# Performance work log

Hardware: AMD Instinct MI355X
Metric: run time of the kernel (lower is better)

The kernel has to match this reference:

```python
import jax, jax.numpy as jnp
import numpy as np

N = 100000
E1 = 600000
E2 = 300000
H = 128
IN = 35
G = 1000
EPS = 1e-5


def _rbf(d):
    # d: [E] distances -> [E, 9] gaussian RBF on [0, 6] with 9 centers
    mu = jnp.linspace(0.0, 6.0, 9, dtype=d.dtype)
    sigma = 6.0 / 9.0
    return jnp.exp(-(((d[:, None] - mu) / sigma) ** 2))


def _bn_eval(x, g, b):
    # BatchNorm1d in eval mode with running_mean=0, running_var=1
    return g * x * (1.0 / np.sqrt(1.0 + EPS)) + b


def _leaky(x):
    return jnp.where(x >= 0, x, 0.01 * x)


def _branch(h, pos, edge_index, cW, cB, nW, nB, g, b):
    row, col = edge_index[0], edge_index[1]
    d = jnp.linalg.norm(pos[row] - pos[col], axis=-1)          # [E]
    radial = jax.nn.silu(_rbf(d) @ cW + cB)                    # [E, H]
    msg = h[row] * radial                                      # gather-mul
    agg = jax.ops.segment_sum(msg, col, num_segments=h.shape[0])  # scatter-add
    return _bn_eval(_leaky((h + agg) @ nW + nB), g, b)


def setup_inputs() -> dict:
    key = jax.random.key(0)
    ks = jax.random.split(key, 16)
    s = lambda fan: 1.0 / np.sqrt(fan)
    inp = {
        "x": jax.random.normal(ks[0], (N, IN), jnp.float32),
        "pos": jax.random.normal(ks[1], (N, 3), jnp.float32) * 2.0,
        "W_in": jax.random.normal(ks[2], (IN, H), jnp.float32) * s(IN),
        "b_in": jnp.zeros((H,), jnp.float32),
        "coordW": jax.random.normal(ks[3], (3, 2, 9, H), jnp.float32) * s(9),
        "coordB": jnp.zeros((3, 2, H), jnp.float32),
        "nodeW": jax.random.normal(ks[4], (3, 2, H, H), jnp.float32) * s(H),
        "nodeB": jnp.zeros((3, 2, H), jnp.float32),
        "bnG": jnp.ones((3, 2, H), jnp.float32),
        "bnB": jnp.zeros((3, 2, H), jnp.float32),
        "fcW": jax.random.normal(ks[5], (3, H, H), jnp.float32) * s(H),
        "fcB": jnp.zeros((3, H), jnp.float32),
        "fcBnG": jnp.ones((3, H), jnp.float32),
        "fcBnB": jnp.zeros((3, H), jnp.float32),
        "outW": jax.random.normal(ks[6], (H, 1), jnp.float32) * s(H),
        "outB": jnp.zeros((1,), jnp.float32),
        "edge_index_intra": jax.random.randint(ks[7], (2, E1), 0, N, jnp.int32),
        "edge_index_inter": jax.random.randint(ks[8], (2, E2), 0, N, jnp.int32),
        "batch": jnp.sort(jax.random.randint(ks[9], (N,), 0, G, jnp.int32)),
    }
    return inp


def reference(x, pos, W_in, b_in, coordW, coordB, nodeW, nodeB, bnG, bnB,
              fcW, fcB, fcBnG, fcBnB, outW, outB,
              edge_index_intra, edge_index_inter, batch):
    h = jax.nn.silu(x @ W_in + b_in)
    for l in range(3):  # 3 GraphInteractionLayers
        intra = _branch(h, pos, edge_index_intra, coordW[l, 0], coordB[l, 0],
                        nodeW[l, 0], nodeB[l, 0], bnG[l, 0], bnB[l, 0])
        inter = _branch(h, pos, edge_index_inter, coordW[l, 1], coordB[l, 1],
                        nodeW[l, 1], nodeB[l, 1], bnG[l, 1], bnB[l, 1])
        h = intra + inter
    hg = jax.ops.segment_sum(h, batch, num_segments=G)  # global_add_pool [G, H]
    for i in range(3):
        hg = _bn_eval(_leaky(hg @ fcW[i] + fcB[i]), fcBnG[i], fcBnB[i])
    out = hg @ outW + outB  # [G, 1]
    return out.reshape(-1)
```

## Files before the change

kernel.cpp:

```cpp
#include <hip/hip_runtime.h>
#include <hip/hip_fp16.h>
#include <math.h>

#define NN   100000
#define HH   128
#define INF_ 35
#define GG   1000
#define LBM  64
#define NBINS 2048
#define DSCALE 128.0f
#define DINV   0.0078125f
#define DCLAMP 15.992f

typedef __attribute__((ext_vector_type(8))) short short8;
typedef __attribute__((ext_vector_type(4))) float f32x4;

static __device__ __forceinline__ float silu_f(float x){ return x / (1.f + __expf(-x)); }
static __device__ __forceinline__ unsigned bf16rne(float x){
    unsigned u = __float_as_uint(x);
    return (u + 0x7FFFu + ((u>>16)&1u)) >> 16;
}
#define BN_INV 0.9999950000374997f

__global__ void k_count(const int* __restrict__ ei1, const int* __restrict__ ei2,
                        int E1, int E2, int n, int* __restrict__ deg){
    int e = blockIdx.x*256 + threadIdx.x;
    int ET = E1 + E2;
    if (e >= ET) return;
    int c;
    if (e < E1) c = ei1[E1 + e];
    else        c = n + ei2[E2 + (e - E1)];
    atomicAdd(&deg[c], 1);
}

__global__ void k_scan1(const int* __restrict__ deg, int n2, int* __restrict__ off, int* __restrict__ bsum){
    __shared__ int s[256];
    int tid = threadIdx.x; int i = blockIdx.x*256 + tid;
    int v = (i<n2)? deg[i] : 0;
    s[tid] = v; __syncthreads();
    for (int ofs=1; ofs<256; ofs<<=1){
        int t = (tid>=ofs)? s[tid-ofs] : 0;
        __syncthreads(); s[tid] += t; __syncthreads();
    }
    if (i<n2) off[i] = s[tid] - v;
    if (tid==255) bsum[blockIdx.x] = s[255];
}

__global__ void k_scan2(int* __restrict__ bsum, int nb){
    __shared__ int s[1024];
    int tid = threadIdx.x;
    int v = (tid<nb)? bsum[tid] : 0;
    s[tid] = v; __syncthreads();
    for (int ofs=1; ofs<1024; ofs<<=1){
        int t = (tid>=ofs)? s[tid-ofs] : 0;
        __syncthreads(); s[tid] += t; __syncthreads();
    }
    if (tid<nb) bsum[tid] = s[tid] - v;
}

__global__ void k_scan3(int* __restrict__ off, const int* __restrict__ bsum, int n2, int ET){
    int i = blockIdx.x*256 + threadIdx.x;
    if (i<n2) off[i] += bsum[i>>8];
    if (i==0) off[n2] = ET;
}

__global__ void k_fill(const int* __restrict__ ei1, const int* __restrict__ ei2,
                       int E1, int E2, int n, const float* __restrict__ pos,
                       const int* __restrict__ off, int* __restrict__ cur,
                       float2* __restrict__ rec){
    int e = blockIdx.x*256 + threadIdx.x;
    int ET = E1 + E2;
    if (e >= ET) return;
    int r, creal, cslot;
    if (e < E1){ r = ei1[e];        creal = ei1[E1 + e];        cslot = creal; }
    else       { int ee = e - E1; r = ei2[ee]; creal = ei2[E2 + ee]; cslot = n + creal; }
    int slot = atomicAdd(&cur[cslot], 1);
    int p = off[cslot] + slot;
    float dx = pos[r*3+0]-pos[creal*3+0];
    float dy = pos[r*3+1]-pos[creal*3+1];
    float dz = pos[r*3+2]-pos[creal*3+2];
    float d  = sqrtf(dx*dx + dy*dy + dz*dz);
    rec[p] = make_float2(__int_as_float(r), d);
}

__global__ void k_prep(const float* __restrict__ nodeW,
                       const float* __restrict__ coordW, const float* __restrict__ coordB,
                       const float* __restrict__ W_in,
                       unsigned short* __restrict__ Bpk, unsigned short* __restrict__ tabs,
                       float* __restrict__ Wtg){
    int blk = blockIdx.x, tx = threadIdx.x;
    if (blk < 48){
        int idx = blk*256 + tx;
        if (idx >= 6*2048) return;
        int li = idx >> 11;
        int r  = idx & 2047;
        int s  = r >> 9;
        int r2 = r & 511;
        int ct = r2 >> 6;
        int l  = r2 & 63;
        const float* src = nodeW + (size_t)li*16384 + (size_t)(s*32 + (l>>4)*8)*HH + ct*16 + (l&15);
        unsigned short o[8];
        #pragma unroll
        for (int j=0;j<8;j++) o[j] = (unsigned short)bf16rne(src[(size_t)j*HH]);
        uint4 v;
        v.x = o[0] | ((unsigned)o[1]<<16);
        v.y = o[2] | ((unsigned)o[3]<<16);
        v.z = o[4] | ((unsigned)o[5]<<16);
        v.w = o[6] | ((unsigned)o[7]<<16);
        *(uint4*)(Bpk + (size_t)idx*8) = v;
    } else if (blk < 66){
        int i = (blk-48)*256 + tx;
        if (i >= 128*36) return;
        int c = i/36, k = i - c*36;
        Wtg[i] = (k < INF_) ? W_in[k*HH + c] : 0.f;
    } else {
        int idx = (blk-66)*256 + tx;
        if (idx >= 6*NBINS*HH) return;
        int li  = idx / (NBINS*HH);
        int rem = idx - li*(NBINS*HH);
        int bin = rem >> 7;
        int col = rem & 127;
        float d0 = (float)bin * DINV;
        float d1 = d0 + DINV;
        const float* cW = coordW + (size_t)li*9*HH;
        float cb = coordB[li*HH + col];
        float q0 = cb, q1 = cb;
        #pragma unroll
        for (int k=0;k<9;k++){
            float wk = cW[k*HH + col];
            float t0 = 1.5f*d0 - 1.125f*(float)k;
            float t1 = 1.5f*d1 - 1.125f*(float)k;
            q0 += __expf(-t0*t0) * wk;
            q1 += __expf(-t1*t1) * wk;
        }
        float v = silu_f(q0);
        float s = silu_f(q1) - v;
        __half hv = __float2half_rn(v);
        __half hs = __float2half_rn(s);
        tabs[(size_t)idx*2+0] = __half_as_ushort(hv);
        tabs[(size_t)idx*2+1] = __half_as_ushort(hs);
    }
}

#define NT_IN (NN/16)
__global__ __launch_bounds__(256) void k_input(const float* __restrict__ x,
        const float* __restrict__ Wtg, const float* __restrict__ b,
        unsigned short* __restrict__ hb){
    __shared__ __align__(16) float xs[16][36];
    int tx = threadIdx.x;
    int c = tx & 127, g = tx >> 7;
    float bc = b[c];
    const float4* wp = (const float4*)(Wtg + c*36);
    for (int tile = blockIdx.x; tile < NT_IN; tile += gridDim.x){
        int r0 = tile*16;
        for (int i = tx; i < 16*INF_; i += 256){
            int rr = i/INF_, kk = i - rr*INF_;
            xs[rr][kk] = x[(size_t)(r0+rr)*INF_ + kk];
        }
        if (tx < 16) xs[tx][35] = 0.f;
        __syncthreads();
        float acc[8];
        #pragma unroll
        for (int j=0;j<8;j++) acc[j] = bc;
        #pragma unroll
        for (int kk=0;kk<9;kk++){
            float4 w4 = wp[kk];
            #pragma unroll
            for (int j=0;j<8;j++){
                float4 xv = *(const float4*)(&xs[g*8+j][kk*4]);
                acc[j] += xv.x*w4.x + xv.y*w4.y + xv.z*w4.z + xv.w*w4.w;
            }
        }
        #pragma unroll
        for (int j=0;j<8;j++){
            int gr = r0 + g*8 + j;
            hb[(size_t)gr*HH + c] = (unsigned short)bf16rne(silu_f(acc[j]));
        }
        __syncthreads();
    }
}

#define GEDGE(RP, S_, B_, F_)                                        \
    int S_ = __float_as_int((RP).x);                                 \
    float db_##S_ = fminf((RP).y, DCLAMP)*DSCALE;                    \
    int B_ = (int)db_##S_; float F_ = db_##S_ - (float)B_;

#define GACC(U_, T_, F_)                                             \
    {                                                                \
        float2 p0 = __half22float2(*(const __half2*)&(T_).x);        \
        float2 p1 = __half22float2(*(const __half2*)&(T_).y);        \
        acc.x += __uint_as_float((U_)<<16)           * (p0.x + p0.y*(F_)); \
        acc.y += __uint_as_float((U_) & 0xFFFF0000u) * (p1.x + p1.y*(F_)); \
    }

__global__ __launch_bounds__(256) void k_gather(
        const unsigned short* __restrict__ hb,
        const int* __restrict__ off, const float2* __restrict__ rec,
        const unsigned short* __restrict__ tab0, const unsigned short* __restrict__ tab1,
        unsigned short* __restrict__ aggb1, unsigned short* __restrict__ aggb2,
        int n, int nblk1){
    int b = blockIdx.x;
    int br = (b >= nblk1) ? 1 : 0;
    int node = (br ? b - nblk1 : b)*4 + (threadIdx.x>>6);
    if (node >= n) return;
    int c = (threadIdx.x & 63)*2;
    const unsigned short* tab = br ? tab1 : tab0;
    unsigned short* aggp = br ? aggb2 : aggb1;

    float2 acc;
    {
        unsigned u = *(const unsigned*)(hb + (size_t)node*HH + c);
        acc.x = __uint_as_float(u<<16); acc.y = __uint_as_float(u & 0xFFFF0000u);
    }

    int slot = node + br*n;
    int lo = off[slot], hi = off[slot+1];
    lo = __builtin_amdgcn_readfirstlane(lo);
    hi = __builtin_amdgcn_readfirstlane(hi);

    int p = lo;
    for (; p+4<=hi; p+=4){
        float2 r0 = rec[p], r1 = rec[p+1], r2 = rec[p+2], r3 = rec[p+3];
        GEDGE(r0, s0, b0, f0)
        GEDGE(r1, s1, b1, f1)
        GEDGE(r2, s2, b2, f2)
        GEDGE(r3, s3, b3, f3)
        unsigned u0 = *(const unsigned*)(hb + (size_t)s0*HH + c);
        unsigned u1 = *(const unsigned*)(hb + (size_t)s1*HH + c);
        unsigned u2 = *(const unsigned*)(hb + (size_t)s2*HH + c);
        unsigned u3 = *(const unsigned*)(hb + (size_t)s3*HH + c);
        uint2 t0 = *(const uint2*)(tab + ((size_t)b0*HH + c)*2);
        uint2 t1 = *(const uint2*)(tab + ((size_t)b1*HH + c)*2);
        uint2 t2 = *(const uint2*)(tab + ((size_t)b2*HH + c)*2);
        uint2 t3 = *(const uint2*)(tab + ((size_t)b3*HH + c)*2);
        GACC(u0, t0, f0)
        GACC(u1, t1, f1)
        GACC(u2, t2, f2)
        GACC(u3, t3, f3)
    }
    for (; p+2<=hi; p+=2){
        float2 r0 = rec[p], r1 = rec[p+1];
        GEDGE(r0, s0, b0, f0)
        GEDGE(r1, s1, b1, f1)
        unsigned u0 = *(const unsigned*)(hb + (size_t)s0*HH + c);
        unsigned u1 = *(const unsigned*)(hb + (size_t)s1*HH + c);
        uint2 t0 = *(const uint2*)(tab + ((size_t)b0*HH + c)*2);
        uint2 t1 = *(const uint2*)(tab + ((size_t)b1*HH + c)*2);
        GACC(u0, t0, f0)
        GACC(u1, t1, f1)
    }
    if (p < hi){
        float2 r0 = rec[p];
        GEDGE(r0, s0, b0, f0)
        unsigned u0 = *(const unsigned*)(hb + (size_t)s0*HH + c);
        uint2 t0 = *(const uint2*)(tab + ((size_t)b0*HH + c)*2);
        GACC(u0, t0, f0)
    }
    unsigned pk = bf16rne(acc.x) | (bf16rne(acc.y)<<16);
    *(unsigned*)(aggp + (size_t)node*HH + c) = pk;
}

__global__ __launch_bounds__(256) void k_gemm2m(
        const unsigned short* __restrict__ A1, const unsigned short* __restrict__ A2,
        const unsigned short* __restrict__ Bp0, const unsigned short* __restrict__ Bp1,
        const float* __restrict__ b1, const float* __restrict__ b2,
        const float* __restrict__ g1, const float* __restrict__ g2,
        const float* __restrict__ e1, const float* __restrict__ e2,
        float* __restrict__ C, unsigned short* __restrict__ Cb, int n){
    int tx = threadIdx.x;
    int l = tx & 63, wv = tx >> 6;
    int rb = blockIdx.x*LBM + wv*16;
    int mlo = l & 15, khi = l >> 4;
    int arow = rb + mlo;
    bool ok = arow < n;

    f32x4 acc0[8], acc1[8];
    #pragma unroll
    for (int ct=0;ct<8;ct++){ acc0[ct] = (f32x4)0.f; acc1[ct] = (f32x4)0.f; }

    {
        short8 af[4];
        const short8* ap = (const short8*)(A1 + (size_t)arow*HH);
        #pragma unroll
        for (int s=0;s<4;s++) af[s] = ok ? ap[s*4 + khi] : (short8)0;
        const short8* bp = (const short8*)Bp0;
        #pragma unroll
        for (int s=0;s<4;s++){
            #pragma unroll
            for (int ct=0;ct<8;ct++){
                short8 bf = bp[s*512 + ct*64 + l];
                acc0[ct] = __builtin_amdgcn_mfma_f32_16x16x32_bf16(af[s], bf, acc0[ct], 0, 0, 0);
            }
        }
    }
    {
        short8 af[4];
        const short8* ap = (const short8*)(A2 + (size_t)arow*HH);
        #pragma unroll
        for (int s=0;s<4;s++) af[s] = ok ? ap[s*4 + khi] : (short8)0;
        const short8* bp = (const short8*)Bp1;
        #pragma unroll
        for (int s=0;s<4;s++){
            #pragma unroll
            for (int ct=0;ct<8;ct++){
                short8 bf = bp[s*512 + ct*64 + l];
                acc1[ct] = __builtin_amdgcn_mfma_f32_16x16x32_bf16(af[s], bf, acc1[ct], 0, 0, 0);
            }
        }
    }

    #pragma unroll
    for (int ct=0;ct<8;ct++){
        int ncol = ct*16 + mlo;
        float bi1 = b1[ncol], ga1 = g1[ncol], bt1 = e1[ncol];
        float bi2 = b2[ncol], ga2 = g2[ncol], bt2 = e2[ncol];
        #pragma unroll
        for (int r=0;r<4;r++){
            int grow = rb + khi*4 + r;
            if (grow < n){
                float xv = acc0[ct][r] + bi1;
                xv = (xv>=0.f)? xv : 0.01f*xv;
                float yv = acc1[ct][r] + bi2;
                yv = (yv>=0.f)? yv : 0.01f*yv;
                float o = (ga1*xv + ga2*yv)*BN_INV + bt1 + bt2;
                if (C) C[(size_t)grow*HH + ncol] = o;
                Cb[(size_t)grow*HH + ncol] = (unsigned short)bf16rne(o);
            }
        }
    }
}

static __device__ __forceinline__ int lower_bound_i(const int* __restrict__ a, int n, int key){
    int lo=0, hi=n;
    while (lo<hi){ int m=(lo+hi)>>1; if (a[m]<key) lo=m+1; else hi=m; }
    return lo;
}
__global__ void k_poolfc(const float* __restrict__ h,
                     const int* __restrict__ batch,
                     const float* __restrict__ fcW, const float* __restrict__ fcB,
                     const float* __restrict__ fbg, const float* __restrict__ fbb,
                     const float* __restrict__ outW, const float* __restrict__ outB,
                     float* __restrict__ out, int n){
    __shared__ float row[HH];
    __shared__ float red[2];
    int g = blockIdx.x, c = threadIdx.x;
    int lo = lower_bound_i(batch, n, g);
    int hi = lower_bound_i(batch, n, g+1);
    float v = 0.f;
    for (int r=lo; r<hi; r++) v += h[(size_t)r*HH + c];
    for (int l=0;l<3;l++){
        row[c] = v; __syncthreads();
        float acc = fcB[l*HH + c];
        const float* W = fcW + (size_t)l*HH*HH;
        #pragma unroll 8
        for (int k=0;k<HH;k++) acc += row[k]*W[k*HH + c];
        acc = (acc>=0.f)? acc : 0.01f*acc;
        v = fbg[l*HH+c]*acc*BN_INV + fbb[l*HH+c];
        __syncthreads();
    }
    float t = v * outW[c];
    #pragma unroll
    for (int o=32;o>0;o>>=1) t += __shfl_down(t, o, 64);
    if ((c&63)==0) red[c>>6] = t;
    __syncthreads();
    if (c==0) out[g] = red[0] + red[1] + outB[0];
}

extern "C" void kernel_launch(void* const* d_in, const int* in_sizes, int n_in,
                              void* d_out, int out_size, void* d_ws, size_t ws_size,
                              hipStream_t stream){
    const float* x      = (const float*)d_in[0];
    const float* pos    = (const float*)d_in[1];
    const float* W_in   = (const float*)d_in[2];
    const float* b_in   = (const float*)d_in[3];
    const float* coordW = (const float*)d_in[4];
    const float* coordB = (const float*)d_in[5];
    const float* nodeW  = (const float*)d_in[6];
    const float* nodeB  = (const float*)d_in[7];
    const float* bnG    = (const float*)d_in[8];
    const float* bnB    = (const float*)d_in[9];
    const float* fcW    = (const float*)d_in[10];
    const float* fcB    = (const float*)d_in[11];
    const float* fcBnG  = (const float*)d_in[12];
    const float* fcBnB  = (const float*)d_in[13];
    const float* outW   = (const float*)d_in[14];
    const float* outB   = (const float*)d_in[15];
    const int* ei1      = (const int*)d_in[16];
    const int* ei2      = (const int*)d_in[17];
    const int* batch    = (const int*)d_in[18];
    const int E1 = in_sizes[16]/2, E2 = in_sizes[17]/2;
    const int n = NN;
    const int n2 = 2*n;
    const int ET = E1 + E2;

    char* w = (char*)d_ws;
    size_t o = 0;
    auto alloc = [&](size_t bytes)->void*{
        void* r = w + o;
        o += (bytes + 255) & ~(size_t)255;
        return r;
    };
    unsigned short* hb    = (unsigned short*)alloc((size_t)n*HH*2);
    unsigned short* hb2   = (unsigned short*)alloc((size_t)n*HH*2);
    unsigned short* aggb1 = (unsigned short*)alloc((size_t)n*HH*2);
    unsigned short* aggb2 = (unsigned short*)alloc((size_t)n*HH*2);
    unsigned short* Bpk   = (unsigned short*)alloc((size_t)6*16384*2);
    unsigned short* tabs  = (unsigned short*)alloc((size_t)6*NBINS*HH*4);
    float*  Wtg  = (float*)alloc((size_t)128*36*4);
    int*    off  = (int*)alloc((size_t)(n2+1)*4);
    int*    cnt  = (int*)alloc((size_t)n2*4);
    int*    cur  = (int*)alloc((size_t)n2*4);
    float2* rec  = (float2*)alloc((size_t)ET*8);
    int*    bsum = (int*)alloc(1024*4);
    float*  hfin = (float*)alloc((size_t)n*HH*4);
    (void)n_in; (void)out_size; (void)ws_size;

    int nb2 = (n2+255)/256;

    hipMemsetAsync(cnt, 0, (size_t)2*n2*4, stream);
    k_count<<<(ET+255)/256,256,0,stream>>>(ei1, ei2, E1, E2, n, cnt);
    k_scan1<<<nb2,256,0,stream>>>(cnt, n2, off, bsum);
    k_scan2<<<1,1024,0,stream>>>(bsum, nb2);
    k_scan3<<<nb2,256,0,stream>>>(off, bsum, n2, ET);
    k_fill<<<(ET+255)/256,256,0,stream>>>(ei1, ei2, E1, E2, n, pos, off, cur, rec);
    k_prep<<<66+6144,256,0,stream>>>(nodeW, coordW, coordB, W_in, Bpk, tabs, Wtg);

    k_input<<<2048,256,0,stream>>>(x, Wtg, b_in, hb);

    int nb4 = (n+3)/4;
    unsigned short* hbcur = hb;
    unsigned short* hboth = hb2;
    for (int l=0; l<3; l++){
        int li0 = l*2, li1 = l*2+1;
        float* Cout = (l==2) ? hfin : nullptr;
        k_gather<<<2*nb4,256,0,stream>>>(hbcur, off, rec,
            tabs + (size_t)li0*NBINS*HH*2, tabs + (size_t)li1*NBINS*HH*2,
            aggb1, aggb2, n, nb4);
        k_gemm2m<<<(n+LBM-1)/LBM,256,0,stream>>>(aggb1, aggb2,
            Bpk + (size_t)li0*16384, Bpk + (size_t)li1*16384,
            nodeB + (size_t)li0*HH,  nodeB + (size_t)li1*HH,
            bnG   + (size_t)li0*HH,  bnG   + (size_t)li1*HH,
            bnB   + (size_t)li0*HH,  bnB   + (size_t)li1*HH,
            Cout, hboth, n);
        unsigned short* tb = hbcur; hbcur = hboth; hboth = tb;
    }

    k_poolfc<<<GG,128,0,stream>>>(hfin, batch, fcW, fcB, fcBnG, fcBnB, outW, outB, (float*)d_out, n);
}
```

Measured before the change: 531.5 us.

## Merge scan into decoupled-lookback kernel, fuse fill with prep, double GEMM rows per wave

The three-pass prefix scan becomes a single-pass scan with decoupled lookback using per-block flags, aggregates and inclusive sums, which the existing memset now also zeroes. The edge fill kernel is merged into the preprocessing kernel as extra blocks, cutting kernel launches from the setup phase. The node GEMM now handles 32 rows per wave (128 per block), reusing each weight fragment for two MFMAs so fewer B loads are issued per output. The lookback spins on earlier blocks and depends on them being scheduled first, and the GEMM change doubles accumulator registers, which may lower occupancy.

Measured after the change: 620.4 us. +16.7%, slower.

```diff
diff --git a/kernel.cpp b/kernel.cpp
--- a/kernel.cpp
+++ b/kernel.cpp
@@ -6,7 +6,7 @@
 #define HH   128
 #define INF_ 35
 #define GG   1000
-#define LBM  64
+#define GBM  128
 #define NBINS 2048
 #define DSCALE 128.0f
 #define DINV   0.0078125f
@@ -33,61 +33,51 @@
     atomicAdd(&deg[c], 1);
 }
 
-__global__ void k_scan1(const int* __restrict__ deg, int n2, int* __restrict__ off, int* __restrict__ bsum){
+__global__ void k_scan_lb(const int* __restrict__ deg, int n2, int* __restrict__ off,
+                          int* __restrict__ agg, int* __restrict__ incl,
+                          unsigned* __restrict__ flags, int ET){
     __shared__ int s[256];
-    int tid = threadIdx.x; int i = blockIdx.x*256 + tid;
+    __shared__ int exc_sh;
+    int blk = blockIdx.x, tid = threadIdx.x;
+    int i = blk*256 + tid;
     int v = (i<n2)? deg[i] : 0;
     s[tid] = v; __syncthreads();
     for (int ofs=1; ofs<256; ofs<<=1){
         int t = (tid>=ofs)? s[tid-ofs] : 0;
         __syncthreads(); s[tid] += t; __syncthreads();
     }
-    if (i<n2) off[i] = s[tid] - v;
-    if (tid==255) bsum[blockIdx.x] = s[255];
-}
-
-__global__ void k_scan2(int* __restrict__ bsum, int nb){
-    __shared__ int s[1024];
-    int tid = threadIdx.x;
-    int v = (tid<nb)? bsum[tid] : 0;
-    s[tid] = v; __syncthreads();
-    for (int ofs=1; ofs<1024; ofs<<=1){
-        int t = (tid>=ofs)? s[tid-ofs] : 0;
-        __syncthreads(); s[tid] += t; __syncthreads();
-    }
-    if (tid<nb) bsum[tid] = s[tid] - v;
-}
-
-__global__ void k_scan3(int* __restrict__ off, const int* __restrict__ bsum, int n2, int ET){
-    int i = blockIdx.x*256 + threadIdx.x;
-    if (i<n2) off[i] += bsum[i>>8];
-    if (i==0) off[n2] = ET;
-}
-
-__global__ void k_fill(const int* __restrict__ ei1, const int* __restrict__ ei2,
-                       int E1, int E2, int n, const float* __restrict__ pos,
-                       const int* __restrict__ off, int* __restrict__ cur,
-                       float2* __restrict__ rec){
-    int e = blockIdx.x*256 + threadIdx.x;
-    int ET = E1 + E2;
-    if (e >= ET) return;
-    int r, creal, cslot;
-    if (e < E1){ r = ei1[e];        creal = ei1[E1 + e];        cslot = creal; }
-    else       { int ee = e - E1; r = ei2[ee]; creal = ei2[E2 + ee]; cslot = n + creal; }
-    int slot = atomicAdd(&cur[cslot], 1);
-    int p = off[cslot] + slot;
-    float dx = pos[r*3+0]-pos[creal*3+0];
-    float dy = pos[r*3+1]-pos[creal*3+1];
-    float dz = pos[r*3+2]-pos[creal*3+2];
-    float d  = sqrtf(dx*dx + dy*dy + dz*dz);
-    rec[p] = make_float2(__int_as_float(r), d);
-}
-
-__global__ void k_prep(const float* __restrict__ nodeW,
-                       const float* __restrict__ coordW, const float* __restrict__ coordB,
-                       const float* __restrict__ W_in,
-                       unsigned short* __restrict__ Bpk, unsigned short* __restrict__ tabs,
-                       float* __restrict__ Wtg){
+    if (tid == 0){
+        int total = s[255];
+        atomicExch(&agg[blk], total);
+        __threadfence();
+        atomicExch(&flags[blk], 1u);
+        int exc = 0;
+        int pb = blk - 1;
+        while (pb >= 0){
+            unsigned f;
+            do { f = atomicAdd(&flags[pb], 0u); } while (f == 0u);
+            if (f == 2u){ exc += atomicAdd(&incl[pb], 0); break; }
+            exc += atomicAdd(&agg[pb], 0);
+            pb--;
+        }
+        atomicExch(&incl[blk], exc + total);
+        __threadfence();
+        atomicExch(&flags[blk], 2u);
+        exc_sh = exc;
+    }
+    __syncthreads();
+    if (i < n2) off[i] = exc_sh + s[tid] - v;
+    if (i == 0) off[n2] = ET;
+}
+
+__global__ void k_build(const float* __restrict__ nodeW,
+                        const float* __restrict__ coordW, const float* __restrict__ coordB,
+                        const float* __restrict__ W_in,
+                        const int* __restrict__ ei1, const int* __restrict__ ei2,
+                        int E1, int E2, int n, const float* __restrict__ pos,
+                        const int* __restrict__ off, int* __restrict__ cur,
+                        unsigned short* __restrict__ Bpk, unsigned short* __restrict__ tabs,
+                        float* __restrict__ Wtg, float2* __restrict__ rec){
     int blk = blockIdx.x, tx = threadIdx.x;
     if (blk < 48){
         int idx = blk*256 + tx;
@@ -113,7 +103,7 @@
         if (i >= 128*36) return;
         int c = i/36, k = i - c*36;
         Wtg[i] = (k < INF_) ? W_in[k*HH + c] : 0.f;
-    } else {
+    } else if (blk < 66+6144){
         int idx = (blk-66)*256 + tx;
         if (idx >= 6*NBINS*HH) return;
         int li  = idx / (NBINS*HH);
@@ -135,10 +125,22 @@
         }
         float v = silu_f(q0);
         float s = silu_f(q1) - v;
-        __half hv = __float2half_rn(v);
-        __half hs = __float2half_rn(s);
-        tabs[(size_t)idx*2+0] = __half_as_ushort(hv);
-        tabs[(size_t)idx*2+1] = __half_as_ushort(hs);
+        tabs[(size_t)idx*2+0] = __half_as_ushort(__float2half_rn(v));
+        tabs[(size_t)idx*2+1] = __half_as_ushort(__float2half_rn(s));
+    } else {
+        int e = (blk - (66+6144))*256 + tx;
+        int ET = E1 + E2;
+        if (e >= ET) return;
+        int r, creal, cslot;
+        if (e < E1){ r = ei1[e];        creal = ei1[E1 + e];        cslot = creal; }
+        else       { int ee = e - E1; r = ei2[ee]; creal = ei2[E2 + ee]; cslot = n + creal; }
+        int slot = atomicAdd(&cur[cslot], 1);
+        int p = off[cslot] + slot;
+        float dx = pos[r*3+0]-pos[creal*3+0];
+        float dy = pos[r*3+1]-pos[creal*3+1];
+        float dz = pos[r*3+2]-pos[creal*3+2];
+        float d  = sqrtf(dx*dx + dy*dy + dz*dz);
+        rec[p] = make_float2(__int_as_float(r), d);
     }
 }
 
@@ -269,42 +271,54 @@
         float* __restrict__ C, unsigned short* __restrict__ Cb, int n){
     int tx = threadIdx.x;
     int l = tx & 63, wv = tx >> 6;
-    int rb = blockIdx.x*LBM + wv*16;
+    int rb = blockIdx.x*GBM + wv*32;
     int mlo = l & 15, khi = l >> 4;
-    int arow = rb + mlo;
-    bool ok = arow < n;
-
-    f32x4 acc0[8], acc1[8];
+    int ar0 = rb + mlo, ar1 = rb + 16 + mlo;
+    bool ok0 = ar0 < n, ok1 = ar1 < n;
+
+    f32x4 accA[2][8], accB[2][8];
     #pragma unroll
-    for (int ct=0;ct<8;ct++){ acc0[ct] = (f32x4)0.f; acc1[ct] = (f32x4)0.f; }
+    for (int rh=0;rh<2;rh++)
+        #pragma unroll
+        for (int ct=0;ct<8;ct++){ accA[rh][ct] = (f32x4)0.f; accB[rh][ct] = (f32x4)0.f; }
 
     {
-        short8 af[4];
-        const short8* ap = (const short8*)(A1 + (size_t)arow*HH);
-        #pragma unroll
-        for (int s=0;s<4;s++) af[s] = ok ? ap[s*4 + khi] : (short8)0;
+        short8 af0[4], af1[4];
+        const short8* ap0 = (const short8*)(A1 + (size_t)ar0*HH);
+        const short8* ap1 = (const short8*)(A1 + (size_t)ar1*HH);
+        #pragma unroll
+        for (int s=0;s<4;s++){
+            af0[s] = ok0 ? ap0[s*4 + khi] : (short8)0;
+            af1[s] = ok1 ? ap1[s*4 + khi] : (short8)0;
+        }
         const short8* bp = (const short8*)Bp0;
         #pragma unroll
         for (int s=0;s<4;s++){
             #pragma unroll
             for (int ct=0;ct<8;ct++){
                 short8 bf = bp[s*512 + ct*64 + l];
-                acc0[ct] = __builtin_amdgcn_mfma_f32_16x16x32_bf16(af[s], bf, acc0[ct], 0, 0, 0);
+                accA[0][ct] = __builtin_amdgcn_mfma_f32_16x16x32_bf16(af0[s], bf, accA[0][ct], 0, 0, 0);
+                accA[1][ct] = __builtin_amdgcn_mfma_f32_16x16x32_bf16(af1[s], bf, accA[1][ct], 0, 0, 0);
             }
         }
     }
     {
-        short8 af[4];
-        const short8* ap = (const short8*)(A2 + (size_t)arow*HH);
-        #pragma unroll
-        for (int s=0;s<4;s++) af[s] = ok ? ap[s*4 + khi] : (short8)0;
+        short8 af0[4], af1[4];
+        const short8* ap0 = (const short8*)(A2 + (size_t)ar0*HH);
+        const short8* ap1 = (const short8*)(A2 + (size_t)ar1*HH);
+        #pragma unroll
+        for (int s=0;s<4;s++){
+            af0[s] = ok0 ? ap0[s*4 + khi] : (short8)0;
+            af1[s] = ok1 ? ap1[s*4 + khi] : (short8)0;
+        }
         const short8* bp = (const short8*)Bp1;
         #pragma unroll
         for (int s=0;s<4;s++){
             #pragma unroll
             for (int ct=0;ct<8;ct++){
                 short8 bf = bp[s*512 + ct*64 + l];
-                acc1[ct] = __builtin_amdgcn_mfma_f32_16x16x32_bf16(af[s], bf, acc1[ct], 0, 0, 0);
+                accB[0][ct] = __builtin_amdgcn_mfma_f32_16x16x32_bf16(af0[s], bf, accB[0][ct], 0, 0, 0);
+                accB[1][ct] = __builtin_amdgcn_mfma_f32_16x16x32_bf16(af1[s], bf, accB[1][ct], 0, 0, 0);
             }
         }
     }
@@ -315,16 +329,19 @@
         float bi1 = b1[ncol], ga1 = g1[ncol], bt1 = e1[ncol];
         float bi2 = b2[ncol], ga2 = g2[ncol], bt2 = e2[ncol];
         #pragma unroll
-        for (int r=0;r<4;r++){
-            int grow = rb + khi*4 + r;
-            if (grow < n){
-                float xv = acc0[ct][r] + bi1;
-                xv = (xv>=0.f)? xv : 0.01f*xv;
-                float yv = acc1[ct][r] + bi2;
-                yv = (yv>=0.f)? yv : 0.01f*yv;
-                float o = (ga1*xv + ga2*yv)*BN_INV + bt1 + bt2;
-                if (C) C[(size_t)grow*HH + ncol] = o;
-                Cb[(size_t)grow*HH + ncol] = (unsigned short)bf16rne(o);
+        for (int rh=0;rh<2;rh++){
+            #pragma unroll
+            for (int r=0;r<4;r++){
+                int grow = rb + rh*16 + khi*4 + r;
+                if (grow < n){
+                    float xv = accA[rh][ct][r] + bi1;
+                    xv = (xv>=0.f)? xv : 0.01f*xv;
+                    float yv = accB[rh][ct][r] + bi2;
+                    yv = (yv>=0.f)? yv : 0.01f*yv;
+                    float o = (ga1*xv + ga2*yv)*BN_INV + bt1 + bt2;
+                    if (C) C[(size_t)grow*HH + ncol] = o;
+                    Cb[(size_t)grow*HH + ncol] = (unsigned short)bf16rne(o);
+                }
             }
         }
     }
@@ -410,20 +427,20 @@
     int*    off  = (int*)alloc((size_t)(n2+1)*4);
     int*    cnt  = (int*)alloc((size_t)n2*4);
     int*    cur  = (int*)alloc((size_t)n2*4);
+    unsigned* flags = (unsigned*)alloc(1024*4);
+    int*    aggl = (int*)alloc(1024*4);
+    int*    incl = (int*)alloc(1024*4);
     float2* rec  = (float2*)alloc((size_t)ET*8);
-    int*    bsum = (int*)alloc(1024*4);
     float*  hfin = (float*)alloc((size_t)n*HH*4);
     (void)n_in; (void)out_size; (void)ws_size;
 
     int nb2 = (n2+255)/256;
 
-    hipMemsetAsync(cnt, 0, (size_t)2*n2*4, stream);
+    hipMemsetAsync(cnt, 0, (size_t)(2*n2 + 1024)*4, stream);
     k_count<<<(ET+255)/256,256,0,stream>>>(ei1, ei2, E1, E2, n, cnt);
-    k_scan1<<<nb2,256,0,stream>>>(cnt, n2, off, bsum);
-    k_scan2<<<1,1024,0,stream>>>(bsum, nb2);
-    k_scan3<<<nb2,256,0,stream>>>(off, bsum, n2, ET);
-    k_fill<<<(ET+255)/256,256,0,stream>>>(ei1, ei2, E1, E2, n, pos, off, cur, rec);
-    k_prep<<<66+6144,256,0,stream>>>(nodeW, coordW, coordB, W_in, Bpk, tabs, Wtg);
+    k_scan_lb<<<nb2,256,0,stream>>>(cnt, n2, off, aggl, incl, flags, ET);
+    k_build<<<66+6144+(ET+255)/256,256,0,stream>>>(nodeW, coordW, coordB, W_in,
+        ei1, ei2, E1, E2, n, pos, off, cur, Bpk, tabs, Wtg, rec);
 
     k_input<<<2048,256,0,stream>>>(x, Wtg, b_in, hb);
 
@@ -436,7 +453,7 @@
         k_gather<<<2*nb4,256,0,stream>>>(hbcur, off, rec,
             tabs + (size_t)li0*NBINS*HH*2, tabs + (size_t)li1*NBINS*HH*2,
             aggb1, aggb2, n, nb4);
-        k_gemm2m<<<(n+LBM-1)/LBM,256,0,stream>>>(aggb1, aggb2,
+        k_gemm2m<<<(n+GBM-1)/GBM,256,0,stream>>>(aggb1, aggb2,
             Bpk + (size_t)li0*16384, Bpk + (size_t)li1*16384,
             nodeB + (size_t)li0*HH,  nodeB + (size_t)li1*HH,
             bnG   + (size_t)li0*HH,  bnG   + (size_t)li1*HH,
```
